# Kernel tuning notes

Hardware: AMD Instinct MI355X
Metric: run time of the kernel (lower is better)

The kernel has to match this reference:

```python
import jax, jax.numpy as jnp
import numpy as np
from math import ceil

B, N, C_IN, H, EDIM = 64, 512, 128, 128, 5
EPG = 16 * N          # edges per graph
E = B * EPG           # 524288 edges total
K1 = ceil(0.5 * N)    # 256 clusters after pool 1
K2 = ceil(0.5 * K1)   # 128 clusters after pool 2
EPS = 1e-15


def dense_mincut_pool(x, adj, s, mask=None):
    # x: [B,n,F], adj: [B,n,n], s: [B,n,k]
    s = jax.nn.softmax(s, axis=-1)
    if mask is not None:
        m = mask[..., None].astype(x.dtype)
        x = x * m
        s = s * m
    out = jnp.einsum('bnk,bnf->bkf', s, x)
    out_adj = jnp.einsum('bnk,bnm,bml->bkl', s, adj, s)
    mincut_num = jnp.trace(out_adj, axis1=-2, axis2=-1)
    d_flat = adj.sum(-1)                                   # degrees [B,n]
    mincut_den = jnp.trace(jnp.einsum('bnk,bn,bnl->bkl', s, d_flat, s), axis1=-2, axis2=-1)
    mincut_loss = jnp.mean(-(mincut_num / mincut_den))
    k = s.shape[-1]
    ss = jnp.einsum('bnk,bnl->bkl', s, s)
    ss_norm = jnp.linalg.norm(ss, axis=(-1, -2), keepdims=True)
    i_s = jnp.eye(k, dtype=x.dtype)
    ortho_loss = jnp.mean(jnp.linalg.norm(ss / ss_norm - i_s / np.sqrt(k), axis=(-1, -2)))
    out_adj = out_adj * (1.0 - i_s)                        # zero diagonal
    d = jnp.sqrt(out_adj.sum(-1))[..., None] + EPS
    out_adj = out_adj / d / jnp.swapaxes(d, -1, -2)
    return out, out_adj, mincut_loss, ortho_loss


def setup_inputs() -> dict:
    key = jax.random.key(0)
    ks = iter(jax.random.split(key, 40))
    NT = B * N
    x = jax.random.normal(next(ks), (NT, C_IN), jnp.float32)
    # within-graph random edges; nodes are sorted by graph (batch = repeat)
    offs = jnp.repeat(jnp.arange(B, dtype=jnp.int32) * N, EPG)
    src = jax.random.randint(next(ks), (E,), 0, N, jnp.int32) + offs
    dst = jax.random.randint(next(ks), (E,), 0, N, jnp.int32) + offs
    edge_index = jnp.stack([src, dst])
    edge_attr = jax.random.normal(next(ks), (E, EDIM), jnp.float32)
    batch = jnp.repeat(jnp.arange(B, dtype=jnp.int32), N)

    def W(shape):
        return jax.random.normal(next(ks), shape, jnp.float32) * 0.05

    inp = dict(x=x, edge_index=edge_index, edge_attr=edge_attr, batch=batch,
               bn_gamma=jnp.ones((C_IN,), jnp.float32), bn_beta=jnp.zeros((C_IN,), jnp.float32),
               Wq=W((C_IN, H)), bq=W((H,)), Wk=W((C_IN, H)), bk=W((H,)),
               Wv=W((C_IN, H)), bv=W((H,)), We=W((EDIM, H)),
               Wskip=W((C_IN, H)), bskip=W((H,)),
               W_mlp1=W((H, K1)), b_mlp1=W((K1,)),
               W2_rel=W((H, H)), b2_rel=W((H,)), W2_root=W((H, H)),
               W_mlp2=W((H, K2)), b_mlp2=W((K2,)),
               W3_rel=W((H, H)), b3_rel=W((H,)), W3_root=W((H, H)),
               W_lin1=W((H, H)), b_lin1=W((H,)),
               W_ro=W((H, 1)), b_ro=W((1,)))
    return inp


def reference(x, edge_index, edge_attr, batch, bn_gamma, bn_beta,
              Wq, bq, Wk, bk, Wv, bv, We, Wskip, bskip,
              W_mlp1, b_mlp1, W2_rel, b2_rel, W2_root,
              W_mlp2, b_mlp2, W3_rel, b3_rel, W3_root,
              W_lin1, b_lin1, W_ro, b_ro):
    NT = x.shape[0]
    # BatchNorm1d (training-mode batch statistics, biased var, eps=1e-5)
    mu = x.mean(0)
    var = x.var(0)
    xh = (x - mu) / jnp.sqrt(var + 1e-5) * bn_gamma + bn_beta

    # TransformerConv (heads=1, concat=True, root_weight=True, edge_dim=5)
    src, dst = edge_index[0], edge_index[1]
    q = xh @ Wq + bq
    k_ = xh @ Wk + bk
    v = xh @ Wv + bv
    e = edge_attr @ We                       # lin_edge has no bias
    kj = k_[src] + e
    vj = v[src] + e
    logits = (q[dst] * kj).sum(-1) / np.sqrt(H)
    m = jax.ops.segment_max(logits, dst, num_segments=NT)
    a = jnp.exp(logits - m[dst])
    denom = jax.ops.segment_sum(a, dst, num_segments=NT)
    alpha = a / denom[dst]
    agg = jax.ops.segment_sum(alpha[:, None] * vj, dst, num_segments=NT)
    h = jax.nn.relu(agg + xh @ Wskip + bskip)

    # to_dense_batch: equal-size graphs sorted by batch -> reshape
    xd = h.reshape(B, N, H)
    mask = jnp.ones((B, N), bool)
    # to_dense_adj: scatter-add edge indicators (duplicates accumulate)
    adj = jnp.zeros((B, N, N), jnp.float32).at[batch[src], src % N, dst % N].add(1.0)

    s = xd @ W_mlp1 + b_mlp1
    xd, adj, mc1, o1 = dense_mincut_pool(xd, adj, s, mask)
    # DenseGraphConv: lin_rel(adj @ x) + lin_root(x)
    xd = jax.nn.relu((adj @ xd) @ W2_rel + b2_rel + xd @ W2_root)
    s = xd @ W_mlp2 + b_mlp2
    xd, adj, mc2, o2 = dense_mincut_pool(xd, adj, s)
    xd = (adj @ xd) @ W3_rel + b3_rel + xd @ W3_root
    g = xd.mean(1)
    g = jax.nn.relu(g @ W_lin1 + b_lin1)
    return jax.nn.sigmoid(g @ W_ro + b_ro).squeeze(-1)   # [B]
```

## Files before the change

kernel.cpp:

```cpp
#include <hip/hip_runtime.h>
#include <math.h>

#define BGRAPH 64
#define NNODE  512
#define NTOT   32768
#define CIN    128
#define HDIM   128
#define EDIM_  5
#define EDGES  524288
#define K1C    256
#define K2C    128

using f32x4 = __attribute__((ext_vector_type(4))) float;
using s16x8 = __attribute__((ext_vector_type(8))) short;

__device__ __forceinline__ short f2bf(float f) {
    union { float f; unsigned u; } v; v.f = f;
    unsigned r = v.u + 0x7fffu + ((v.u >> 16) & 1u);
    return (short)(r >> 16);
}
__device__ __forceinline__ float bf2f(short s) {
    union { unsigned u; float f; } v; v.u = ((unsigned)(unsigned short)s) << 16;
    return v.f;
}

__global__ __launch_bounds__(256) void prep_kernel(const float* __restrict__ x,
                                                   float* __restrict__ psum,
                                                   float* __restrict__ psq,
                                                   const float* __restrict__ Wq, const float* __restrict__ Wk,
                                                   const float* __restrict__ Wv, const float* __restrict__ Ws,
                                                   const float* __restrict__ bq, const float* __restrict__ bk,
                                                   const float* __restrict__ bv, const float* __restrict__ bs,
                                                   float* __restrict__ W4, float* __restrict__ bias4,
                                                   const int* __restrict__ ei,
                                                   int* __restrict__ deg_src,
                                                   int* __restrict__ deg_dst) {
    __shared__ float ss[128], sq[128];
    int tid = threadIdx.x, bid = blockIdx.x;
    if (bid < 256) {
        long idx0 = (long)bid * 256 + tid;
        float4 s = {0.f, 0.f, 0.f, 0.f}, q = {0.f, 0.f, 0.f, 0.f};
#pragma unroll
        for (int it = 0; it < 16; ++it) {
            float4 v = *(const float4*)(x + (idx0 + (long)it * 65536) * 4);
            s.x += v.x; s.y += v.y; s.z += v.z; s.w += v.w;
            q.x += v.x * v.x; q.y += v.y * v.y; q.z += v.z * v.z; q.w += v.w * v.w;
        }
        if (tid < 128) { ss[tid] = 0.f; sq[tid] = 0.f; }
        __syncthreads();
        int c0 = (tid & 31) * 4;
        atomicAdd(&ss[c0 + 0], s.x); atomicAdd(&ss[c0 + 1], s.y);
        atomicAdd(&ss[c0 + 2], s.z); atomicAdd(&ss[c0 + 3], s.w);
        atomicAdd(&sq[c0 + 0], q.x); atomicAdd(&sq[c0 + 1], q.y);
        atomicAdd(&sq[c0 + 2], q.z); atomicAdd(&sq[c0 + 3], q.w);
        __syncthreads();
        if (tid < 128) {
            psum[bid * 128 + tid] = ss[tid];
            psq[bid * 128 + tid]  = sq[tid];
        }
    } else if (bid < 512) {
        int i = (bid - 256) * 256 + tid;
        if (i < 128 * 512) {
            int k = i / 512, j = i % 512;
            float v;
            if (j < 128)      v = Wq[k * 128 + j];
            else if (j < 256) v = Wk[k * 128 + (j - 128)];
            else if (j < 384) v = Wv[k * 128 + (j - 256)];
            else              v = Ws[k * 128 + (j - 384)];
            W4[i] = v;
        }
        if (i < 512) {
            float v;
            if (i < 128)      v = bq[i];
            else if (i < 256) v = bk[i - 128];
            else if (i < 384) v = bv[i - 256];
            else              v = bs[i - 384];
            bias4[i] = v;
        }
    } else {
        int e = (bid - 512) * 256 + tid;
        if (e < EDGES) {
            atomicAdd(&deg_src[ei[e]], 1);
            atomicAdd(&deg_dst[ei[EDGES + e]], 1);
        }
    }
}

__global__ __launch_bounds__(1024) void scan2fin_kernel(const int* __restrict__ deg_src,
                                                        int* __restrict__ rp_src, int* __restrict__ cur_src,
                                                        const int* __restrict__ deg_dst,
                                                        int* __restrict__ rp_dst, int* __restrict__ cur_dst,
                                                        const float* __restrict__ psum,
                                                        const float* __restrict__ psq,
                                                        const float* __restrict__ gamma,
                                                        const float* __restrict__ beta,
                                                        float* __restrict__ scale,
                                                        float* __restrict__ shift,
                                                        float* __restrict__ gsum) {
    __shared__ int part[1024];
    int tid = threadIdx.x;
    if (blockIdx.x == 2) {
        if (tid < 128) {
            int c = tid;
            float s = 0.f, q = 0.f;
            for (int b = 0; b < 256; ++b) { s += psum[b * 128 + c]; q += psq[b * 128 + c]; }
            float mu  = s / (float)NTOT;
            float var = q / (float)NTOT - mu * mu;
            float rstd = rsqrtf(var + 1e-5f);
            float sc = gamma[c] * rstd;
            scale[c] = sc;
            shift[c] = beta[c] - mu * sc;
        }
        for (int i = tid; i < BGRAPH * 128; i += 1024) gsum[i] = 0.f;
        return;
    }
    const int* deg = blockIdx.x ? deg_dst : deg_src;
    int* rowptr    = blockIdx.x ? rp_dst  : rp_src;
    int* cursor    = blockIdx.x ? cur_dst : cur_src;
    int base = tid * 32;
    int s = 0;
    for (int i = 0; i < 32; ++i) s += deg[base + i];
    part[tid] = s;
    __syncthreads();
    for (int off = 1; off < 1024; off <<= 1) {
        int v = part[tid];
        int add = (tid >= off) ? part[tid - off] : 0;
        __syncthreads();
        part[tid] = v + add;
        __syncthreads();
    }
    int run = (tid == 0) ? 0 : part[tid - 1];
    for (int i = 0; i < 32; ++i) {
        rowptr[base + i] = run;
        cursor[base + i] = run;
        run += deg[base + i];
    }
}

template <int TILE, bool TRANS_A, bool AFFINE, bool ANORM, bool ROWSUM, bool RELU,
          bool DUAL, bool OBF16, bool AU8, bool BBF16, bool ATRBF16, bool ABF16>
__device__ __forceinline__ void mgemm_body(short* As, short* Bs, float* dvl,
                                           const void* __restrict__ Av,
                                           const void* __restrict__ Bv,
                                           const void* __restrict__ A2v,
                                           const void* __restrict__ B2v,
                                           int Ksplit,
                                           const float* __restrict__ bias,
                                           void* __restrict__ Cv,
                                           const float* __restrict__ scale,
                                           const float* __restrict__ shift,
                                           int M, int Nc, int K,
                                           int lda, int ldb, int ldc,
                                           long sA, long sB, long sC,
                                           int bx, int by, int bz) {
    constexpr int ASZ = AU8 ? 1 : ((ATRBF16 || ABF16) ? 2 : 4);
    constexpr int BSZ = BBF16 ? 2 : 4;
    const char* Abase = (const char*)Av + (long)bz * sA * ASZ;
    const char* Bbase = (const char*)Bv + (long)bz * sB * BSZ;
    float* C = (float*)Cv + (OBF16 ? 0 : (long)bz * sC);
    short* Cs = (short*)Cv + (OBF16 ? (long)bz * sC : 0);
    const int m0 = by * TILE, n0 = bx * TILE;
    const int tid = threadIdx.x;
    const int lane16 = tid & 15;
    const int quad = (tid & 63) >> 4;
    const int wrow = (tid >> 6) >> 1, wcol = (tid >> 6) & 1;
    constexpr int WT = TILE / 32;

    if (ANORM) {
        for (int i = tid; i < K; i += 256)
            dvl[i] = 1.f / (sqrtf(scale[(long)bz * lda + i]) + 1e-15f);
        __syncthreads();
    }

    f32x4 acc[WT][WT] = {};

    for (int k0 = 0; k0 < K; k0 += 32) {
        const char* Au = Abase; const char* Bu = Bbase; int ku = k0;
        if (DUAL && k0 >= Ksplit) { Au = (const char*)A2v; Bu = (const char*)B2v; ku = k0 - Ksplit; }

        if (!TRANS_A) {
#pragma unroll
            for (int p = 0; p < TILE / 32; ++p) {
                int idx = tid + p * 256;
                int row = idx >> 3, c4 = idx & 7;
                short4 o;
                if (AU8) {
                    unsigned u = *(const unsigned*)((const unsigned char*)Au +
                                                    (long)(m0 + row) * lda + ku + c4 * 4);
                    o = make_short4(f2bf((float)(u & 255u)), f2bf((float)((u >> 8) & 255u)),
                                    f2bf((float)((u >> 16) & 255u)), f2bf((float)((u >> 24) & 255u)));
                } else if (ABF16) {
                    o = *(const short4*)((const short*)Au + (long)(m0 + row) * lda + ku + c4 * 4);
                } else {
                    float4 v = *(const float4*)((const float*)Au + (long)(m0 + row) * lda + ku + c4 * 4);
                    if (AFFINE) {
                        int k = ku + c4 * 4;
                        v.x = v.x * scale[k] + shift[k];
                        v.y = v.y * scale[k + 1] + shift[k + 1];
                        v.z = v.z * scale[k + 2] + shift[k + 2];
                        v.w = v.w * scale[k + 3] + shift[k + 3];
                    }
                    if (ANORM) {
                        int k = ku + c4 * 4;
                        int grow = m0 + row;
                        float dr = dvl[grow];
                        v.x = (grow == k + 0) ? 0.f : v.x * dr * dvl[k + 0];
                        v.y = (grow == k + 1) ? 0.f : v.y * dr * dvl[k + 1];
                        v.z = (grow == k + 2) ? 0.f : v.z * dr * dvl[k + 2];
                        v.w = (grow == k + 3) ? 0.f : v.w * dr * dvl[k + 3];
                    }
                    o = make_short4(f2bf(v.x), f2bf(v.y), f2bf(v.z), f2bf(v.w));
                }
                *(short4*)&As[row * 40 + c4 * 4] = o;
            }
        } else {
            if (TILE == 128 || tid < 128) {
                int c4 = tid >> 3, g = tid & 7;
                short* d = &As[(c4 * 4) * 40 + g * 4];
                if (ATRBF16) {
                    const short* src = (const short*)Au + (long)(ku + g * 4) * lda + m0 + c4 * 4;
                    short4 r0 = *(const short4*)(src);
                    short4 r1 = *(const short4*)(src + lda);
                    short4 r2 = *(const short4*)(src + 2 * lda);
                    short4 r3 = *(const short4*)(src + 3 * lda);
                    *(short4*)(d + 0 * 40) = make_short4(r0.x, r1.x, r2.x, r3.x);
                    *(short4*)(d + 1 * 40) = make_short4(r0.y, r1.y, r2.y, r3.y);
                    *(short4*)(d + 2 * 40) = make_short4(r0.z, r1.z, r2.z, r3.z);
                    *(short4*)(d + 3 * 40) = make_short4(r0.w, r1.w, r2.w, r3.w);
                } else {
                    const float* src = (const float*)Au + (long)(ku + g * 4) * lda + m0 + c4 * 4;
                    float4 r0 = *(const float4*)(src);
                    float4 r1 = *(const float4*)(src + lda);
                    float4 r2 = *(const float4*)(src + 2 * lda);
                    float4 r3 = *(const float4*)(src + 3 * lda);
                    *(short4*)(d + 0 * 40) = make_short4(f2bf(r0.x), f2bf(r1.x), f2bf(r2.x), f2bf(r3.x));
                    *(short4*)(d + 1 * 40) = make_short4(f2bf(r0.y), f2bf(r1.y), f2bf(r2.y), f2bf(r3.y));
                    *(short4*)(d + 2 * 40) = make_short4(f2bf(r0.z), f2bf(r1.z), f2bf(r2.z), f2bf(r3.z));
                    *(short4*)(d + 3 * 40) = make_short4(f2bf(r0.w), f2bf(r1.w), f2bf(r2.w), f2bf(r3.w));
                }
            }
        }
        if (TILE == 128 || tid < 128) {
            int c4 = tid >> 3, g = tid & 7;
            short* d = &Bs[(c4 * 4) * 40 + g * 4];
            if (BBF16) {
                const short* src = (const short*)Bu + (long)(ku + g * 4) * ldb + n0 + c4 * 4;
                short4 r0 = *(const short4*)(src);
                short4 r1 = *(const short4*)(src + ldb);
                short4 r2 = *(const short4*)(src + 2 * ldb);
                short4 r3 = *(const short4*)(src + 3 * ldb);
                *(short4*)(d + 0 * 40) = make_short4(r0.x, r1.x, r2.x, r3.x);
                *(short4*)(d + 1 * 40) = make_short4(r0.y, r1.y, r2.y, r3.y);
                *(short4*)(d + 2 * 40) = make_short4(r0.z, r1.z, r2.z, r3.z);
                *(short4*)(d + 3 * 40) = make_short4(r0.w, r1.w, r2.w, r3.w);
            } else {
                const float* src = (const float*)Bu + (long)(ku + g * 4) * ldb + n0 + c4 * 4;
                float4 r0 = *(const float4*)(src);
                float4 r1 = *(const float4*)(src + ldb);
                float4 r2 = *(const float4*)(src + 2 * ldb);
                float4 r3 = *(const float4*)(src + 3 * ldb);
                *(short4*)(d + 0 * 40) = make_short4(f2bf(r0.x), f2bf(r1.x), f2bf(r2.x), f2bf(r3.x));
                *(short4*)(d + 1 * 40) = make_short4(f2bf(r0.y), f2bf(r1.y), f2bf(r2.y), f2bf(r3.y));
                *(short4*)(d + 2 * 40) = make_short4(f2bf(r0.z), f2bf(r1.z), f2bf(r2.z), f2bf(r3.z));
                *(short4*)(d + 3 * 40) = make_short4(f2bf(r0.w), f2bf(r1.w), f2bf(r2.w), f2bf(r3.w));
            }
        }
        __syncthreads();

        s16x8 af[WT], bf[WT];
#pragma unroll
        for (int t = 0; t < WT; ++t) {
            af[t] = *(const s16x8*)&As[(wrow * (TILE / 2) + t * 16 + lane16) * 40 + quad * 8];
            bf[t] = *(const s16x8*)&Bs[(wcol * (TILE / 2) + t * 16 + lane16) * 40 + quad * 8];
        }
#pragma unroll
        for (int i = 0; i < WT; ++i)
#pragma unroll
            for (int j = 0; j < WT; ++j)
                acc[i][j] = __builtin_amdgcn_mfma_f32_16x16x32_bf16(af[i], bf[j], acc[i][j], 0, 0, 0);
        __syncthreads();
    }

#pragma unroll
    for (int i = 0; i < WT; ++i) {
        int gm = m0 + wrow * (TILE / 2) + i * 16 + quad * 4;
#pragma unroll
        for (int j = 0; j < WT; ++j) {
            int gn = n0 + wcol * (TILE / 2) + j * 16 + lane16;
            float bv = bias ? bias[gn] : 0.f;
#pragma unroll
            for (int r = 0; r < 4; ++r) {
                float val = acc[i][j][r] + bv;
                if (RELU) val = fmaxf(val, 0.f);
                if (OBF16) Cs[(long)(gm + r) * ldc + gn] = f2bf(val);
                else       C[(long)(gm + r) * ldc + gn] = val;
            }
        }
    }

    if (ROWSUM) {
        float* rlA = (float*)As;
        float* rlB = (float*)Bs;
#pragma unroll
        for (int i = 0; i < WT; ++i) {
#pragma unroll
            for (int r = 0; r < 4; ++r) {
                int gm = m0 + wrow * (TILE / 2) + i * 16 + quad * 4 + r;
                float p = 0.f;
#pragma unroll
                for (int j = 0; j < WT; ++j) {
                    int gn = n0 + wcol * (TILE / 2) + j * 16 + lane16;
                    p += (gn == gm) ? 0.f : acc[i][j][r];
                }
#pragma unroll
                for (int off = 1; off < 16; off <<= 1) p += __shfl_xor(p, off);
                if (lane16 == 0) {
                    int rl = wrow * (TILE / 2) + i * 16 + quad * 4 + r;
                    (wcol ? rlB : rlA)[rl] = p;
                }
            }
        }
        __syncthreads();
        float* rout = (float*)shift;
        for (int t = tid; t < TILE; t += 256)
            atomicAdd(&rout[(long)bz * M + m0 + t], rlA[t] + rlB[t]);
    }
}

template <int TILE, bool TRANS_A, bool AFFINE, bool ANORM, bool ROWSUM, bool RELU,
          bool DUAL, bool OBF16, bool AU8, bool BBF16, bool ATRBF16, bool ABF16>
__global__ __launch_bounds__(256) void mgemm(const void* __restrict__ Av,
                                             const void* __restrict__ Bv,
                                             const void* __restrict__ A2v,
                                             const void* __restrict__ B2v,
                                             int Ksplit,
                                             const float* __restrict__ bias,
                                             void* __restrict__ Cv,
                                             const float* __restrict__ scale,
                                             const float* __restrict__ shift,
                                             int M, int Nc, int K,
                                             int lda, int ldb, int ldc,
                                             long sA, long sB, long sC) {
    __shared__ __align__(16) short As[TILE * 40];
    __shared__ __align__(16) short Bs[TILE * 40];
    __shared__ float dvl[ANORM ? 256 : 1];
    mgemm_body<TILE, TRANS_A, AFFINE, ANORM, ROWSUM, RELU, DUAL, OBF16, AU8, BBF16, ATRBF16, ABF16>(
        As, Bs, dvl, Av, Bv, A2v, B2v, Ksplit, bias, Cv, scale, shift,
        M, Nc, K, lda, ldb, ldc, sA, sB, sC,
        blockIdx.x, blockIdx.y, blockIdx.z);
}

__global__ __launch_bounds__(256) void qkvs_scatter_kernel(const float* __restrict__ x,
                                                           const float* __restrict__ W4,
                                                           const float* __restrict__ bias4,
                                                           short* __restrict__ qkvs,
                                                           const float* __restrict__ scale,
                                                           const float* __restrict__ shift,
                                                           const int* __restrict__ ei,
                                                           int* __restrict__ cur_src,
                                                           int* __restrict__ cur_dst,
                                                           int* __restrict__ eid_src,
                                                           int* __restrict__ eid_dst) {
    __shared__ __align__(16) short As[128 * 40];
    __shared__ __align__(16) short Bs[128 * 40];
    int b = blockIdx.x;
    if (b < 1024) {
        mgemm_body<128, false, true, false, false, false, false, true, false, false, false, false>(
            As, Bs, nullptr, x, W4, nullptr, nullptr, 0, bias4, qkvs, scale, shift,
            NTOT, 512, 128, 128, 512, 512, 0, 0, 0,
            b & 3, b >> 2, 0);
    } else {
        int e = (b - 1024) * 256 + threadIdx.x;
        if (e < EDGES) {
            int s = ei[e], d = ei[EDGES + e];
            eid_src[atomicAdd(&cur_src[s], 1)] = e;
            eid_dst[atomicAdd(&cur_dst[d], 1)] = e;
        }
    }
}

__global__ __launch_bounds__(256) void pool1_kernel(const short* __restrict__ s1b,
                                                    const short* __restrict__ h,
                                                    const short* __restrict__ T1s,
                                                    float* __restrict__ xp1,
                                                    float* __restrict__ adj1,
                                                    float* __restrict__ rowsum1) {
    __shared__ __align__(16) short As[128 * 40];
    __shared__ __align__(16) short Bs[128 * 40];
    int b = blockIdx.x;
    if (b < 512) {
        mgemm_body<64, true, false, false, false, false, false, false, false, true, true, false>(
            As, Bs, nullptr, s1b, h, nullptr, nullptr, 0, nullptr, xp1, nullptr, nullptr,
            K1C, 128, NNODE, K1C, 128, 128,
            (long)NNODE * K1C, (long)NNODE * 128, (long)K1C * 128,
            b & 1, (b >> 1) & 3, b >> 3);
    } else {
        int j = b - 512;
        mgemm_body<128, true, false, false, true, false, false, false, false, true, true, false>(
            As, Bs, nullptr, s1b, T1s, nullptr, nullptr, 0, nullptr, adj1, nullptr, rowsum1,
            K1C, K1C, NNODE, K1C, K1C, K1C,
            (long)NNODE * K1C, (long)NNODE * K1C, (long)K1C * K1C,
            j & 1, (j >> 1) & 1, j >> 2);
    }
}

__global__ __launch_bounds__(256) void pool2_kernel(const float* __restrict__ adj1,
                                                    const float* __restrict__ rowsum1,
                                                    const short* __restrict__ s2b,
                                                    const short* __restrict__ xd2,
                                                    float* __restrict__ t2,
                                                    float* __restrict__ xp2) {
    __shared__ __align__(16) short As[64 * 40];
    __shared__ __align__(16) short Bs[64 * 40];
    __shared__ float dvl[256];
    int b = blockIdx.x;
    if (b < 512) {
        mgemm_body<64, false, false, true, false, false, false, false, false, true, false, false>(
            As, Bs, dvl, adj1, s2b, nullptr, nullptr, 0, nullptr, t2, rowsum1, nullptr,
            K1C, K2C, K1C, K1C, K2C, K2C,
            (long)K1C * K1C, (long)K1C * K2C, (long)K1C * K2C,
            b & 1, (b >> 1) & 3, b >> 3);
    } else {
        int j = b - 512;
        mgemm_body<64, true, false, false, false, false, false, false, false, true, true, false>(
            As, Bs, nullptr, s2b, xd2, nullptr, nullptr, 0, nullptr, xp2, nullptr, nullptr,
            K2C, 128, K1C, K2C, 128, 128,
            (long)K1C * K2C, (long)K1C * 128, (long)K2C * 128,
            j & 1, (j >> 1) & 1, j >> 2);
    }
}

template <int KADJ, bool RELU, bool OBF16, bool COLSUM>
__global__ __launch_bounds__(256) void fused_gc_kernel(const float* __restrict__ adj,
                                                       const float* __restrict__ rowsum,
                                                       const float* __restrict__ xp,
                                                       const float* __restrict__ Wrel,
                                                       const float* __restrict__ brel,
                                                       const float* __restrict__ Wroot,
                                                       void* __restrict__ Outv) {
    __shared__ __align__(16) short As[64 * 40];
    __shared__ __align__(16) short Bs[128 * 40];
    __shared__ __align__(16) short Tl[64][136];
    __shared__ float dvl[KADJ];
    __shared__ float cs[COLSUM ? 128 : 1];
    const int z = blockIdx.y;
    const int m0 = blockIdx.x * 64;
    const int tid = threadIdx.x;
    const int lane16 = tid & 15;
    const int quad = (tid & 63) >> 4;
    const int wrow = (tid >> 6) >> 1, wcol = (tid >> 6) & 1;
    const float* adjz = adj + (long)z * KADJ * KADJ;
    const float* xpz  = xp + (long)z * KADJ * 128;

    for (int i = tid; i < KADJ; i += 256)
        dvl[i] = 1.f / (sqrtf(rowsum[(long)z * KADJ + i]) + 1e-15f);
    if (COLSUM) for (int i = tid; i < 128; i += 256) cs[i] = 0.f;
    __syncthreads();

    f32x4 acc[2][4] = {};
    for (int k0 = 0; k0 < KADJ; k0 += 32) {
#pragma unroll
        for (int p = 0; p < 2; ++p) {
            int idx = tid + p * 256;
            int row = idx >> 3, c4 = idx & 7;
            int grow = m0 + row, k = k0 + c4 * 4;
            float4 v = *(const float4*)(adjz + (long)grow * KADJ + k);
            float dr = dvl[grow];
            v.x = (grow == k + 0) ? 0.f : v.x * dr * dvl[k + 0];
            v.y = (grow == k + 1) ? 0.f : v.y * dr * dvl[k + 1];
            v.z = (grow == k + 2) ? 0.f : v.z * dr * dvl[k + 2];
            v.w = (grow == k + 3) ? 0.f : v.w * dr * dvl[k + 3];
            *(short4*)&As[row * 40 + c4 * 4] =
                make_short4(f2bf(v.x), f2bf(v.y), f2bf(v.z), f2bf(v.w));
        }
        {
            int c4 = tid >> 3, g = tid & 7;
            short* d = &Bs[(c4 * 4) * 40 + g * 4];
            const float* src = xpz + (long)(k0 + g * 4) * 128 + c4 * 4;
            float4 r0 = *(const float4*)(src);
            float4 r1 = *(const float4*)(src + 128);
            float4 r2 = *(const float4*)(src + 256);
            float4 r3 = *(const float4*)(src + 384);
            *(short4*)(d + 0 * 40) = make_short4(f2bf(r0.x), f2bf(r1.x), f2bf(r2.x), f2bf(r3.x));
            *(short4*)(d + 1 * 40) = make_short4(f2bf(r0.y), f2bf(r1.y), f2bf(r2.y), f2bf(r3.y));
            *(short4*)(d + 2 * 40) = make_short4(f2bf(r0.z), f2bf(r1.z), f2bf(r2.z), f2bf(r3.z));
            *(short4*)(d + 3 * 40) = make_short4(f2bf(r0.w), f2bf(r1.w), f2bf(r2.w), f2bf(r3.w));
        }
        __syncthreads();
        s16x8 af[2], bf[4];
#pragma unroll
        for (int t = 0; t < 2; ++t)
            af[t] = *(const s16x8*)&As[(wrow * 32 + t * 16 + lane16) * 40 + quad * 8];
#pragma unroll
        for (int j = 0; j < 4; ++j)
            bf[j] = *(const s16x8*)&Bs[(wcol * 64 + j * 16 + lane16) * 40 + quad * 8];
#pragma unroll
        for (int t = 0; t < 2; ++t)
#pragma unroll
            for (int j = 0; j < 4; ++j)
                acc[t][j] = __builtin_amdgcn_mfma_f32_16x16x32_bf16(af[t], bf[j], acc[t][j], 0, 0, 0);
        __syncthreads();
    }
#pragma unroll
    for (int t = 0; t < 2; ++t)
#pragma unroll
        for (int j = 0; j < 4; ++j)
#pragma unroll
            for (int r = 0; r < 4; ++r)
                Tl[wrow * 32 + t * 16 + quad * 4 + r][wcol * 64 + j * 16 + lane16] =
                    f2bf(acc[t][j][r]);
    __syncthreads();

    f32x4 acc2[2][4] = {};
    for (int k0 = 0; k0 < 256; k0 += 32) {
        const bool useXp = (k0 >= 128);
        const float* Wsrc = useXp ? (Wroot + (long)(k0 - 128) * 128)
                                  : (Wrel + (long)k0 * 128);
        {
            int c4 = tid >> 3, g = tid & 7;
            short* d = &Bs[(c4 * 4) * 40 + g * 4];
            const float* src = Wsrc + (long)(g * 4) * 128 + c4 * 4;
            float4 r0 = *(const float4*)(src);
            float4 r1 = *(const float4*)(src + 128);
            float4 r2 = *(const float4*)(src + 256);
            float4 r3 = *(const float4*)(src + 384);
            *(short4*)(d + 0 * 40) = make_short4(f2bf(r0.x), f2bf(r1.x), f2bf(r2.x), f2bf(r3.x));
            *(short4*)(d + 1 * 40) = make_short4(f2bf(r0.y), f2bf(r1.y), f2bf(r2.y), f2bf(r3.y));
            *(short4*)(d + 2 * 40) = make_short4(f2bf(r0.z), f2bf(r1.z), f2bf(r2.z), f2bf(r3.z));
            *(short4*)(d + 3 * 40) = make_short4(f2bf(r0.w), f2bf(r1.w), f2bf(r2.w), f2bf(r3.w));
        }
        if (useXp) {
#pragma unroll
            for (int p = 0; p < 2; ++p) {
                int idx = tid + p * 256;
                int row = idx >> 3, c4 = idx & 7;
                float4 v = *(const float4*)(xpz + (long)(m0 + row) * 128 + (k0 - 128) + c4 * 4);
                *(short4*)&As[row * 40 + c4 * 4] =
                    make_short4(f2bf(v.x), f2bf(v.y), f2bf(v.z), f2bf(v.w));
            }
        }
        __syncthreads();
        s16x8 af[2], bf[4];
#pragma unroll
        for (int t = 0; t < 2; ++t) {
            int ar = wrow * 32 + t * 16 + lane16;
            af[t] = useXp ? *(const s16x8*)&As[ar * 40 + quad * 8]
                          : *(const s16x8*)&Tl[ar][k0 + quad * 8];
        }
#pragma unroll
        for (int j = 0; j < 4; ++j)
            bf[j] = *(const s16x8*)&Bs[(wcol * 64 + j * 16 + lane16) * 40 + quad * 8];
#pragma unroll
        for (int t = 0; t < 2; ++t)
#pragma unroll
            for (int j = 0; j < 4; ++j)
                acc2[t][j] = __builtin_amdgcn_mfma_f32_16x16x32_bf16(af[t], bf[j], acc2[t][j], 0, 0, 0);
        __syncthreads();
    }

    if (!COLSUM) {
        float* Of = (float*)Outv;
        short* Ob = (short*)Outv;
#pragma unroll
        for (int t = 0; t < 2; ++t) {
#pragma unroll
            for (int j = 0; j < 4; ++j) {
                int gcol = wcol * 64 + j * 16 + lane16;
                float bv = brel[gcol];
#pragma unroll
                for (int r = 0; r < 4; ++r) {
                    int grow = m0 + wrow * 32 + t * 16 + quad * 4 + r;
                    float val = acc2[t][j][r] + bv;
                    if (RELU) val = fmaxf(val, 0.f);
                    long oi = ((long)z * KADJ + grow) * 128 + gcol;
                    if (OBF16) Ob[oi] = f2bf(val);
                    else       Of[oi] = val;
                }
            }
        }
    } else {
#pragma unroll
        for (int j = 0; j < 4; ++j) {
            int gcol = wcol * 64 + j * 16 + lane16;
            float bv = brel[gcol];
            float p = 0.f;
#pragma unroll
            for (int t = 0; t < 2; ++t)
#pragma unroll
                for (int r = 0; r < 4; ++r) {
                    float val = acc2[t][j][r] + bv;
                    if (RELU) val = fmaxf(val, 0.f);
                    p += val;
                }
            atomicAdd(&cs[gcol], p);
        }
        __syncthreads();
        float* gsum = (float*)Outv;
        for (int i = tid; i < 128; i += 256)
            atomicAdd(&gsum[(long)z * 128 + i], cs[i]);
    }
}

template <int NC>
__global__ __launch_bounds__(256) void mlp_softmax_kernel(const short* __restrict__ A,
                                                          const float* __restrict__ W,
                                                          const float* __restrict__ bias,
                                                          short* __restrict__ Out) {
    __shared__ __align__(16) short As[64 * 40];
    __shared__ __align__(16) short Ws[NC * 40];
    const int tid = threadIdx.x;
    const int lane16 = tid & 15;
    const int quad = (tid & 63) >> 4;
    const int wv = tid >> 6;
    const int m0 = blockIdx.x * 64;
    constexpr int NT = NC / 16;

    f32x4 acc[NT] = {};

    for (int k0 = 0; k0 < 128; k0 += 32) {
        {
            int row = tid >> 2, g = tid & 3;
            *(s16x8*)&As[row * 40 + g * 8] =
                *(const s16x8*)(A + (long)(m0 + row) * 128 + k0 + g * 8);
        }
#pragma unroll
        for (int p = 0; p < NC / 128; ++p) {
            int c4 = tid >> 3, g = tid & 7;
            int n0 = p * 128 + c4 * 4;
            short* d = &Ws[n0 * 40 + g * 4];
            const float* src = W + (long)(k0 + g * 4) * NC + n0;
            float4 r0 = *(const float4*)(src);
            float4 r1 = *(const float4*)(src + NC);
            float4 r2 = *(const float4*)(src + 2 * NC);
            float4 r3 = *(const float4*)(src + 3 * NC);
            *(short4*)(d + 0 * 40) = make_short4(f2bf(r0.x), f2bf(r1.x), f2bf(r2.x), f2bf(r3.x));
            *(short4*)(d + 1 * 40) = make_short4(f2bf(r0.y), f2bf(r1.y), f2bf(r2.y), f2bf(r3.y));
            *(short4*)(d + 2 * 40) = make_short4(f2bf(r0.z), f2bf(r1.z), f2bf(r2.z), f2bf(r3.z));
            *(short4*)(d + 3 * 40) = make_short4(f2bf(r0.w), f2bf(r1.w), f2bf(r2.w), f2bf(r3.w));
        }
        __syncthreads();

        s16x8 af = *(const s16x8*)&As[(wv * 16 + lane16) * 40 + quad * 8];
#pragma unroll
        for (int t = 0; t < NT; ++t) {
            s16x8 bf = *(const s16x8*)&Ws[(t * 16 + lane16) * 40 + quad * 8];
            acc[t] = __builtin_amdgcn_mfma_f32_16x16x32_bf16(af, bf, acc[t], 0, 0, 0);
        }
        __syncthreads();
    }

    float mx[4] = {-INFINITY, -INFINITY, -INFINITY, -INFINITY};
#pragma unroll
    for (int t = 0; t < NT; ++t) {
        float bv = bias[t * 16 + lane16];
#pragma unroll
        for (int r = 0; r < 4; ++r) {
            float x = bf2f(f2bf(acc[t][r] + bv));
            acc[t][r] = x;
            mx[r] = fmaxf(mx[r], x);
        }
    }
#pragma unroll
    for (int off = 8; off; off >>= 1)
#pragma unroll
        for (int r = 0; r < 4; ++r) mx[r] = fmaxf(mx[r], __shfl_xor(mx[r], off));
    float sm[4] = {0.f, 0.f, 0.f, 0.f};
#pragma unroll
    for (int t = 0; t < NT; ++t)
#pragma unroll
        for (int r = 0; r < 4; ++r) {
            float e = expf(acc[t][r] - mx[r]);
            acc[t][r] = e;
            sm[r] += e;
        }
#pragma unroll
    for (int off = 8; off; off >>= 1)
#pragma unroll
        for (int r = 0; r < 4; ++r) sm[r] += __shfl_xor(sm[r], off);
#pragma unroll
    for (int r = 0; r < 4; ++r) sm[r] = 1.f / sm[r];
#pragma unroll
    for (int t = 0; t < NT; ++t)
#pragma unroll
        for (int r = 0; r < 4; ++r)
            Out[(long)(m0 + wv * 16 + quad * 4 + r) * NC + t * 16 + lane16] =
                f2bf(acc[t][r] * sm[r]);
}

template <bool OBF16>
__global__ __launch_bounds__(256) void bgemm(const short* __restrict__ A,
                                             const short* __restrict__ B,
                                             void* __restrict__ Cv,
                                             float outscale,
                                             int M, int Nc, int K,
                                             int lda, int ldb, int ldc,
                                             long sA, long sB, long sC) {
    __shared__ __align__(16) short As[128 * 40];
    __shared__ __align__(16) short Bs[128 * 40];
    int L = blockIdx.x + (blockIdx.y << 2) + (blockIdx.z << 4);
    int xcd = L & 7, i = L >> 3;
    const int z = xcd * 8 + (i >> 4);
    const int m0 = ((i >> 2) & 3) * 128, n0 = (i & 3) * 128;
    A += (long)z * sA;
    B += (long)z * sB;
    float* C = (float*)Cv + (OBF16 ? 0 : (long)z * sC);
    short* Cs = (short*)Cv + (OBF16 ? (long)z * sC : 0);
    const int tid = threadIdx.x;
    const int lane16 = tid & 15;
    const int quad = (tid & 63) >> 4;
    const int wrow = (tid >> 6) >> 1, wcol = (tid >> 6) & 1;

    f32x4 acc[4][4] = {};

    for (int k0 = 0; k0 < K; k0 += 32) {
#pragma unroll
        for (int p = 0; p < 2; ++p) {
            int u = tid + p * 256;
            int row = u >> 2, g = u & 3;
            *(s16x8*)&As[row * 40 + g * 8] =
                *(const s16x8*)(A + (long)(m0 + row) * lda + k0 + g * 8);
        }
#pragma unroll
        for (int p = 0; p < 2; ++p) {
            int u = tid + p * 256;
            int row = u >> 2, g = u & 3;
            *(s16x8*)&Bs[row * 40 + g * 8] =
                *(const s16x8*)(B + (long)(n0 + row) * ldb + k0 + g * 8);
        }
        __syncthreads();

        s16x8 af[4], bf[4];
#pragma unroll
        for (int t = 0; t < 4; ++t) {
            af[t] = *(const s16x8*)&As[(wrow * 64 + t * 16 + lane16) * 40 + quad * 8];
            bf[t] = *(const s16x8*)&Bs[(wcol * 64 + t * 16 + lane16) * 40 + quad * 8];
        }
#pragma unroll
        for (int i2 = 0; i2 < 4; ++i2)
#pragma unroll
            for (int j = 0; j < 4; ++j)
                acc[i2][j] = __builtin_amdgcn_mfma_f32_16x16x32_bf16(af[i2], bf[j], acc[i2][j], 0, 0, 0);
        __syncthreads();
    }

#pragma unroll
    for (int i2 = 0; i2 < 4; ++i2) {
        int gm = m0 + wrow * 64 + i2 * 16 + quad * 4;
#pragma unroll
        for (int j = 0; j < 4; ++j) {
            int gn = n0 + wcol * 64 + j * 16 + lane16;
#pragma unroll
            for (int r = 0; r < 4; ++r) {
                float val = acc[i2][j][r] * outscale;
                if (OBF16) Cs[(long)(gm + r) * ldc + gn] = f2bf(val);
                else       C[(long)(gm + r) * ldc + gn] = val;
            }
        }
    }
}

__global__ __launch_bounds__(256) void attn_pv_kernel(const short* __restrict__ S,
                                                      const int* __restrict__ ei,
                                                      const float* __restrict__ eattr,
                                                      const float* __restrict__ We,
                                                      const int* __restrict__ rp_dst,
                                                      const int* __restrict__ deg_dst,
                                                      const int* __restrict__ eid_dst,
                                                      const short* __restrict__ qkvs,
                                                      float* __restrict__ alpha,
                                                      short* __restrict__ h) {
    __shared__ float sWe[EDIM_ * 128];
    __shared__ __align__(16) short sS[16][528];
    int g = threadIdx.x >> 4;
    int lane = threadIdx.x & 15;
    int gbase = (threadIdx.x & 63) & ~15;
    int b = blockIdx.x;
    int xcd = b & 7, idx = b >> 3;
    int nb = (xcd * 8 + (idx >> 5)) * 32 + (idx & 31);
    int node = nb * 16 + g;

    {
        const short* Srow = S + (long)node * 512;
        short* Sl = sS[g];
#pragma unroll
        for (int j = 0; j < 4; ++j)
            *(s16x8*)&Sl[j * 128 + lane * 8] = *(const s16x8*)(Srow + j * 128 + lane * 8);
    }
    for (int i = threadIdx.x; i < EDIM_ * 128; i += 256) sWe[i] = We[i];
    __syncthreads();
    const short* Sl = sS[g];

    float qw[EDIM_];
    {
        s16x8 qv = *(const s16x8*)(qkvs + (long)node * 512 + lane * 8);
        float qf[8];
#pragma unroll
        for (int j = 0; j < 8; ++j) qf[j] = bf2f(qv[j]);
#pragma unroll
        for (int d = 0; d < EDIM_; ++d) {
            float p = 0.f;
#pragma unroll
            for (int j = 0; j < 8; ++j) p += qf[j] * sWe[d * 128 + lane * 8 + j];
            qw[d] = p;
        }
#pragma unroll
        for (int off = 8; off; off >>= 1)
#pragma unroll
            for (int d = 0; d < EDIM_; ++d) qw[d] += __shfl_xor(qw[d], off);
#pragma unroll
        for (int d = 0; d < EDIM_; ++d) qw[d] *= 0.08838834764831845f;
    }

    int start = rp_dst[node], cnt = deg_dst[node];
    int nch = (cnt + 15) >> 4;

    float lsum = 0.f, a5[EDIM_] = {};
    int   src_c[4] = {0, 0, 0, 0};
    float a_c[4]   = {0.f, 0.f, 0.f, 0.f};
    for (int c = 0; c < nch; ++c) {
        int t = c * 16 + lane;
        int src = 0; float wv = 0.f;
        if (t < cnt) {
            int e = eid_dst[start + t];
            src = ei[e];
            float lg = bf2f(Sl[src & 511]);
            float ea[EDIM_];
#pragma unroll
            for (int d = 0; d < EDIM_; ++d) { ea[d] = eattr[e * EDIM_ + d]; lg += ea[d] * qw[d]; }
            wv = expf(lg);
            lsum += wv;
#pragma unroll
            for (int d = 0; d < EDIM_; ++d) a5[d] += wv * ea[d];
        }
        if (c < 4) { src_c[c] = src; a_c[c] = wv; }
        else if (t < cnt) alpha[start + t] = wv;
    }
#pragma unroll
    for (int off = 8; off; off >>= 1) {
        lsum += __shfl_xor(lsum, off);
#pragma unroll
        for (int d = 0; d < EDIM_; ++d) a5[d] += __shfl_xor(a5[d], off);
    }
    float inv = (lsum > 0.f) ? 1.f / lsum : 0.f;
    float e5[EDIM_];
#pragma unroll
    for (int d = 0; d < EDIM_; ++d) e5[d] = a5[d] * inv;

    float acc[8] = {};
    for (int c = 0; c < nch; ++c) {
        int src; float a;
        if (c < 4) { src = src_c[c]; a = a_c[c]; }
        else {
            int t = c * 16 + lane;
            if (t < cnt) {
                int e = eid_dst[start + t];
                src = ei[e];
                a = alpha[start + t];
            } else { src = 0; a = 0.f; }
        }
        int m = min(16, cnt - c * 16);
        if (m == 16) {
#pragma unroll
            for (int j = 0; j < 16; ++j) {
                int   sj = __shfl(src, gbase + j);
                float aj = __shfl(a,   gbase + j);
                s16x8 v = *(const s16x8*)(qkvs + (long)sj * 512 + 256 + lane * 8);
#pragma unroll
                for (int k = 0; k < 8; ++k) acc[k] += aj * bf2f(v[k]);
            }
        } else {
            for (int j = 0; j < m; ++j) {
                int   sj = __shfl(src, gbase + j);
                float aj = __shfl(a,   gbase + j);
                s16x8 v = *(const s16x8*)(qkvs + (long)sj * 512 + 256 + lane * 8);
#pragma unroll
                for (int k = 0; k < 8; ++k) acc[k] += aj * bf2f(v[k]);
            }
        }
    }

    s16x8 sk = *(const s16x8*)(qkvs + (long)node * 512 + 384 + lane * 8);
    s16x8 o;
#pragma unroll
    for (int j = 0; j < 8; ++j) {
        float ec = 0.f;
#pragma unroll
        for (int d = 0; d < EDIM_; ++d) ec += e5[d] * sWe[d * 128 + lane * 8 + j];
        float val = acc[j] * inv + ec + bf2f(sk[j]);
        o[j] = f2bf(fmaxf(val, 0.f));
    }
    *(s16x8*)(h + (long)node * 128 + lane * 8) = o;
}

__global__ __launch_bounds__(256) void t1_gather_kernel(const int* __restrict__ ei,
                                                        const int* __restrict__ rp_src,
                                                        const int* __restrict__ deg_src,
                                                        const int* __restrict__ eid_src,
                                                        const short* __restrict__ s1b,
                                                        short* __restrict__ T1s) {
    int g = threadIdx.x >> 4;
    int lane = threadIdx.x & 15;
    int gbase = (threadIdx.x & 63) & ~15;
    int b = blockIdx.x;
    int xcd = b & 7, idx = b >> 3;
    int nb = (xcd * 8 + (idx >> 5)) * 32 + (idx & 31);
    int node = nb * 16 + g;

    int start = rp_src[node], cnt = deg_src[node];
    int nch = (cnt + 15) >> 4;
    float acc[16] = {};
    for (int c = 0; c < nch; ++c) {
        int t = c * 16 + lane;
        int dst = 0;
        if (t < cnt) {
            int e = eid_src[start + t];
            dst = ei[EDGES + e];
        }
        int m = min(16, cnt - c * 16);
        if (m == 16) {
#pragma unroll
            for (int j = 0; j < 16; ++j) {
                int dj = __shfl(dst, gbase + j);
                const s16x8* p = (const s16x8*)(s1b + (long)dj * 256 + lane * 16);
                s16x8 v0 = p[0], v1 = p[1];
#pragma unroll
                for (int k = 0; k < 8; ++k) { acc[k] += bf2f(v0[k]); acc[8 + k] += bf2f(v1[k]); }
            }
        } else {
            for (int j = 0; j < m; ++j) {
                int dj = __shfl(dst, gbase + j);
                const s16x8* p = (const s16x8*)(s1b + (long)dj * 256 + lane * 16);
                s16x8 v0 = p[0], v1 = p[1];
#pragma unroll
                for (int k = 0; k < 8; ++k) { acc[k] += bf2f(v0[k]); acc[8 + k] += bf2f(v1[k]); }
            }
        }
    }
    s16x8 o0, o1;
#pragma unroll
    for (int k = 0; k < 8; ++k) { o0[k] = f2bf(acc[k]); o1[k] = f2bf(acc[8 + k]); }
    short* o = T1s + (long)node * 256 + lane * 16;
    *(s16x8*)(o)     = o0;
    *(s16x8*)(o + 8) = o1;
}

__global__ __launch_bounds__(128) void readout_kernel(const float* __restrict__ gsum,
                                                      const float* __restrict__ W_lin1,
                                                      const float* __restrict__ b_lin1,
                                                      const float* __restrict__ W_ro,
                                                      const float* __restrict__ b_ro,
                                                      float* __restrict__ out) {
    int b = blockIdx.x, t = threadIdx.x;
    __shared__ float g[128], g2[128], wred[2];
    g[t] = gsum[(long)b * 128 + t] * (1.f / (float)K2C);
    __syncthreads();
    float u = b_lin1[t];
    for (int k = 0; k < 128; ++k) u += g[k] * W_lin1[k * 128 + t];
    g2[t] = fmaxf(u, 0.f);
    __syncthreads();
    float p = g2[t] * W_ro[t];
#pragma unroll
    for (int off = 32; off; off >>= 1) p += __shfl_xor(p, off);
    if ((t & 63) == 0) wred[t >> 6] = p;
    __syncthreads();
    if (t == 0) {
        float tot = wred[0] + wred[1] + b_ro[0];
        out[b] = 1.f / (1.f + expf(-tot));
    }
}

extern "C" void kernel_launch(void* const* d_in, const int* in_sizes, int n_in,
                              void* d_out, int out_size, void* d_ws, size_t ws_size,
                              hipStream_t stream) {
    const float* x      = (const float*)d_in[0];
    const int*   ei     = (const int*)d_in[1];
    const float* eattr  = (const float*)d_in[2];
    const float* gamma  = (const float*)d_in[4];
    const float* beta   = (const float*)d_in[5];
    const float* Wq     = (const float*)d_in[6];
    const float* bq     = (const float*)d_in[7];
    const float* Wk     = (const float*)d_in[8];
    const float* bk     = (const float*)d_in[9];
    const float* Wv     = (const float*)d_in[10];
    const float* bv     = (const float*)d_in[11];
    const float* We     = (const float*)d_in[12];
    const float* Wskip  = (const float*)d_in[13];
    const float* bskip  = (const float*)d_in[14];
    const float* W_mlp1 = (const float*)d_in[15];
    const float* b_mlp1 = (const float*)d_in[16];
    const float* W2_rel = (const float*)d_in[17];
    const float* b2_rel = (const float*)d_in[18];
    const float* W2_root= (const float*)d_in[19];
    const float* W_mlp2 = (const float*)d_in[20];
    const float* b_mlp2 = (const float*)d_in[21];
    const float* W3_rel = (const float*)d_in[22];
    const float* b3_rel = (const float*)d_in[23];
    const float* W3_root= (const float*)d_in[24];
    const float* W_lin1 = (const float*)d_in[25];
    const float* b_lin1 = (const float*)d_in[26];
    const float* W_ro   = (const float*)d_in[27];
    const float* b_ro   = (const float*)d_in[28];
    float* out = (float*)d_out;

    char* w = (char*)d_ws;
    const size_t MB = 1ull << 20;
    short* qkvs = (short*)(w + 0);
    short* S    = (short*)(w + 32 * MB);
    short* T1s  = (short*)(w + 48 * MB);
    short* s1b  = (short*)(w + 64 * MB);
    short* xd2  = (short*)(w + 56 * MB);
    short* s2b  = (short*)(w + 72 * MB);
    float* t2   = (float*)(w + 64 * MB);
    float* adj2 = (float*)(w + 0);
    float* xp2  = (float*)(w + 4 * MB);
    float* adj1 = (float*)(w + 80 * MB);
    float* xp1  = (float*)(w + 96 * MB);
    float* alpha= (float*)(w + 97 * MB);
    short* h    = (short*)(w + 112 * MB);
    char* misc  = w + 104 * MB;
    float* W4     = (float*)(misc + 0x00000);
    float* bias4  = (float*)(misc + 0x40000);
    float* scale  = (float*)(misc + 0x41400);
    float* shift  = (float*)(misc + 0x41600);
    float* rowsum1= (float*)(misc + 0x42000);
    float* rowsum2= (float*)(misc + 0x52000);
    int* deg_src  = (int*)(misc + 0x60000);
    int* deg_dst  = (int*)(misc + 0x80000);
    int* rp_src   = (int*)(misc + 0xA0000);
    int* rp_dst   = (int*)(misc + 0xC0000);
    int* cur_src  = (int*)(misc + 0xE0000);
    int* cur_dst  = (int*)(misc + 0x100000);
    int* eid_src  = (int*)(misc + 0x120000);
    int* eid_dst  = (int*)(misc + 0x320000);
    float* psum   = (float*)(misc + 0x520000);
    float* psq    = (float*)(misc + 0x540000);
    float* gsum   = (float*)(misc + 0x560000);

    hipMemsetAsync(misc + 0x42000, 0, 0xA0000 - 0x42000, stream);

    prep_kernel<<<2560, 256, 0, stream>>>(x, psum, psq,
                                          Wq, Wk, Wv, Wskip, bq, bk, bv, bskip,
                                          W4, bias4, ei, deg_src, deg_dst);

    scan2fin_kernel<<<3, 1024, 0, stream>>>(deg_src, rp_src, cur_src,
                                            deg_dst, rp_dst, cur_dst,
                                            psum, psq, gamma, beta, scale, shift, gsum);

    qkvs_scatter_kernel<<<3072, 256, 0, stream>>>(x, W4, bias4, qkvs, scale, shift,
                                                  ei, cur_src, cur_dst, eid_src, eid_dst);

    bgemm<true><<<dim3(4, 4, BGRAPH), 256, 0, stream>>>(
        qkvs + 0, qkvs + 128, S, 0.08838834764831845f,
        NNODE, NNODE, 128, 512, 512, 512,
        (long)NNODE * 512, (long)NNODE * 512, (long)NNODE * NNODE);

    attn_pv_kernel<<<NTOT / 16, 256, 0, stream>>>(
        S, ei, eattr, We, rp_dst, deg_dst, eid_dst, qkvs, alpha, h);

    mlp_softmax_kernel<K1C><<<NTOT / 64, 256, 0, stream>>>(h, W_mlp1, b_mlp1, s1b);

    t1_gather_kernel<<<NTOT / 16, 256, 0, stream>>>(
        ei, rp_src, deg_src, eid_src, s1b, T1s);

    pool1_kernel<<<768, 256, 0, stream>>>(s1b, h, T1s, xp1, adj1, rowsum1);

    fused_gc_kernel<K1C, true, true, false><<<dim3(4, BGRAPH), 256, 0, stream>>>(
        adj1, rowsum1, xp1, W2_rel, b2_rel, W2_root, xd2);

    mlp_softmax_kernel<K2C><<<(BGRAPH * K1C) / 64, 256, 0, stream>>>(xd2, W_mlp2, b_mlp2, s2b);

    pool2_kernel<<<768, 256, 0, stream>>>(adj1, rowsum1, s2b, xd2, t2, xp2);

    mgemm<64, true, false, false, true, false, false, false, false, false, true, false>
        <<<dim3(2, 2, BGRAPH), 256, 0, stream>>>(
        s2b, t2, nullptr, nullptr, 0, nullptr, adj2, nullptr, rowsum2,
        K2C, K2C, K1C, K2C, K2C, K2C,
        (long)K1C * K2C, (long)K1C * K2C, (long)K2C * K2C);

    fused_gc_kernel<K2C, false, false, true><<<dim3(2, BGRAPH), 256, 0, stream>>>(
        adj2, rowsum2, xp2, W3_rel, b3_rel, W3_root, gsum);

    readout_kernel<<<BGRAPH, 128, 0, stream>>>(gsum, W_lin1, b_lin1, W_ro, b_ro, out);

    (void)in_sizes; (void)n_in; (void)out_size; (void)ws_size;
}
```

Measured before the change: 444.5 us.

## Build per-graph CSR in shared memory instead of global atomics and scans

Removes the global degree-count atomics, the global prefix-scan kernel and the global cursor atomics used to build src/dst CSR. Each graph's edges are now bucketed in one block, using shared-memory counting, a block scan and a local scatter, and this work runs alongside the QKVS GEMM blocks. This relies on edges being contiguous per graph with nodes local to each graph, and it changes edge ordering within each row to a nondeterministic one. It also shrinks the memset and the prep grid.

```diff
diff --git a/kernel.cpp b/kernel.cpp
--- a/kernel.cpp
+++ b/kernel.cpp
@@ -8,6 +8,7 @@
 #define HDIM   128
 #define EDIM_  5
 #define EDGES  524288
+#define EPG    8192
 #define K1C    256
 #define K2C    128
 
@@ -31,10 +32,7 @@
                                                    const float* __restrict__ Wv, const float* __restrict__ Ws,
                                                    const float* __restrict__ bq, const float* __restrict__ bk,
                                                    const float* __restrict__ bv, const float* __restrict__ bs,
-                                                   float* __restrict__ W4, float* __restrict__ bias4,
-                                                   const int* __restrict__ ei,
-                                                   int* __restrict__ deg_src,
-                                                   int* __restrict__ deg_dst) {
+                                                   float* __restrict__ W4, float* __restrict__ bias4) {
     __shared__ float ss[128], sq[128];
     int tid = threadIdx.x, bid = blockIdx.x;
     if (bid < 256) {
@@ -58,7 +56,7 @@
             psum[bid * 128 + tid] = ss[tid];
             psq[bid * 128 + tid]  = sq[tid];
         }
-    } else if (bid < 512) {
+    } else {
         int i = (bid - 256) * 256 + tid;
         if (i < 128 * 512) {
             int k = i / 512, j = i % 512;
@@ -77,64 +75,29 @@
             else              v = bs[i - 384];
             bias4[i] = v;
         }
-    } else {
-        int e = (bid - 512) * 256 + tid;
-        if (e < EDGES) {
-            atomicAdd(&deg_src[ei[e]], 1);
-            atomicAdd(&deg_dst[ei[EDGES + e]], 1);
-        }
-    }
-}
-
-__global__ __launch_bounds__(1024) void scan2fin_kernel(const int* __restrict__ deg_src,
-                                                        int* __restrict__ rp_src, int* __restrict__ cur_src,
-                                                        const int* __restrict__ deg_dst,
-                                                        int* __restrict__ rp_dst, int* __restrict__ cur_dst,
-                                                        const float* __restrict__ psum,
-                                                        const float* __restrict__ psq,
-                                                        const float* __restrict__ gamma,
-                                                        const float* __restrict__ beta,
-                                                        float* __restrict__ scale,
-                                                        float* __restrict__ shift,
-                                                        float* __restrict__ gsum) {
-    __shared__ int part[1024];
+    }
+}
+
+__global__ __launch_bounds__(1024) void fin_kernel(const float* __restrict__ psum,
+                                                   const float* __restrict__ psq,
+                                                   const float* __restrict__ gamma,
+                                                   const float* __restrict__ beta,
+                                                   float* __restrict__ scale,
+                                                   float* __restrict__ shift,
+                                                   float* __restrict__ gsum) {
     int tid = threadIdx.x;
-    if (blockIdx.x == 2) {
-        if (tid < 128) {
-            int c = tid;
-            float s = 0.f, q = 0.f;
-            for (int b = 0; b < 256; ++b) { s += psum[b * 128 + c]; q += psq[b * 128 + c]; }
-            float mu  = s / (float)NTOT;
-            float var = q / (float)NTOT - mu * mu;
-            float rstd = rsqrtf(var + 1e-5f);
-            float sc = gamma[c] * rstd;
-            scale[c] = sc;
-            shift[c] = beta[c] - mu * sc;
-        }
-        for (int i = tid; i < BGRAPH * 128; i += 1024) gsum[i] = 0.f;
-        return;
-    }
-    const int* deg = blockIdx.x ? deg_dst : deg_src;
-    int* rowptr    = blockIdx.x ? rp_dst  : rp_src;
-    int* cursor    = blockIdx.x ? cur_dst : cur_src;
-    int base = tid * 32;
-    int s = 0;
-    for (int i = 0; i < 32; ++i) s += deg[base + i];
-    part[tid] = s;
-    __syncthreads();
-    for (int off = 1; off < 1024; off <<= 1) {
-        int v = part[tid];
-        int add = (tid >= off) ? part[tid - off] : 0;
-        __syncthreads();
-        part[tid] = v + add;
-        __syncthreads();
-    }
-    int run = (tid == 0) ? 0 : part[tid - 1];
-    for (int i = 0; i < 32; ++i) {
-        rowptr[base + i] = run;
-        cursor[base + i] = run;
-        run += deg[base + i];
-    }
+    if (tid < 128) {
+        int c = tid;
+        float s = 0.f, q = 0.f;
+        for (int b = 0; b < 256; ++b) { s += psum[b * 128 + c]; q += psq[b * 128 + c]; }
+        float mu  = s / (float)NTOT;
+        float var = q / (float)NTOT - mu * mu;
+        float rstd = rsqrtf(var + 1e-5f);
+        float sc = gamma[c] * rstd;
+        scale[c] = sc;
+        shift[c] = beta[c] - mu * sc;
+    }
+    for (int i = tid; i < BGRAPH * 128; i += 1024) gsum[i] = 0.f;
 }
 
 template <int TILE, bool TRANS_A, bool AFFINE, bool ANORM, bool ROWSUM, bool RELU,
@@ -350,32 +313,82 @@
         blockIdx.x, blockIdx.y, blockIdx.z);
 }
 
-__global__ __launch_bounds__(256) void qkvs_scatter_kernel(const float* __restrict__ x,
-                                                           const float* __restrict__ W4,
-                                                           const float* __restrict__ bias4,
-                                                           short* __restrict__ qkvs,
-                                                           const float* __restrict__ scale,
-                                                           const float* __restrict__ shift,
-                                                           const int* __restrict__ ei,
-                                                           int* __restrict__ cur_src,
-                                                           int* __restrict__ cur_dst,
-                                                           int* __restrict__ eid_src,
-                                                           int* __restrict__ eid_dst) {
-    __shared__ __align__(16) short As[128 * 40];
-    __shared__ __align__(16) short Bs[128 * 40];
+__device__ __forceinline__ void csr_build_graph(int* smemInt,
+                                                const int* __restrict__ ei_dir,
+                                                int gnode0, int gedge0,
+                                                int* __restrict__ rp,
+                                                int* __restrict__ deg,
+                                                int* __restrict__ eid) {
+    int* cnt  = smemInt;
+    int* part = smemInt + 512;
+    int* eidl = smemInt + 768;
+    int tid = threadIdx.x;
+    cnt[tid] = 0; cnt[tid + 256] = 0;
+    __syncthreads();
+    for (int k = 0; k < EPG / 256; ++k) {
+        int e = gedge0 + k * 256 + tid;
+        atomicAdd(&cnt[ei_dir[e] & 511], 1);
+    }
+    __syncthreads();
+    int c0 = cnt[2 * tid], c1 = cnt[2 * tid + 1];
+    part[tid] = c0 + c1;
+    __syncthreads();
+    for (int off = 1; off < 256; off <<= 1) {
+        int v = part[tid];
+        int add = (tid >= off) ? part[tid - off] : 0;
+        __syncthreads();
+        part[tid] = v + add;
+        __syncthreads();
+    }
+    int excl = (tid == 0) ? 0 : part[tid - 1];
+    rp[gnode0 + 2 * tid]      = gedge0 + excl;
+    rp[gnode0 + 2 * tid + 1]  = gedge0 + excl + c0;
+    deg[gnode0 + 2 * tid]     = c0;
+    deg[gnode0 + 2 * tid + 1] = c1;
+    cnt[2 * tid]     = excl;
+    cnt[2 * tid + 1] = excl + c0;
+    __syncthreads();
+    for (int k = 0; k < EPG / 256; ++k) {
+        int e = gedge0 + k * 256 + tid;
+        int pos = atomicAdd(&cnt[ei_dir[e] & 511], 1);
+        eidl[pos] = e;
+    }
+    __syncthreads();
+    for (int k = 0; k < EPG / 256; ++k)
+        eid[gedge0 + k * 256 + tid] = eidl[k * 256 + tid];
+}
+
+__global__ __launch_bounds__(256) void qkvs_csr_kernel(const float* __restrict__ x,
+                                                       const float* __restrict__ W4,
+                                                       const float* __restrict__ bias4,
+                                                       short* __restrict__ qkvs,
+                                                       const float* __restrict__ scale,
+                                                       const float* __restrict__ shift,
+                                                       const int* __restrict__ ei,
+                                                       int* __restrict__ rp_src,
+                                                       int* __restrict__ deg_src,
+                                                       int* __restrict__ eid_src,
+                                                       int* __restrict__ rp_dst,
+                                                       int* __restrict__ deg_dst,
+                                                       int* __restrict__ eid_dst) {
+    __shared__ __align__(16) char smem[35840];
     int b = blockIdx.x;
     if (b < 1024) {
+        short* As = (short*)smem;
+        short* Bs = (short*)(smem + 10240);
         mgemm_body<128, false, true, false, false, false, false, true, false, false, false, false>(
             As, Bs, nullptr, x, W4, nullptr, nullptr, 0, bias4, qkvs, scale, shift,
             NTOT, 512, 128, 128, 512, 512, 0, 0, 0,
             b & 3, b >> 2, 0);
     } else {
-        int e = (b - 1024) * 256 + threadIdx.x;
-        if (e < EDGES) {
-            int s = ei[e], d = ei[EDGES + e];
-            eid_src[atomicAdd(&cur_src[s], 1)] = e;
-            eid_dst[atomicAdd(&cur_dst[d], 1)] = e;
-        }
+        int j = b - 1024;
+        int g = j >> 1;
+        if (j & 1)
+            csr_build_graph((int*)smem, ei + EDGES, g * NNODE, g * EPG,
+                            rp_dst, deg_dst, eid_dst);
+        else
+            csr_build_graph((int*)smem, ei, g * NNODE, g * EPG,
+                            rp_src, deg_src, eid_src);
     }
 }
 
@@ -1028,26 +1041,23 @@
     int* deg_dst  = (int*)(misc + 0x80000);
     int* rp_src   = (int*)(misc + 0xA0000);
     int* rp_dst   = (int*)(misc + 0xC0000);
-    int* cur_src  = (int*)(misc + 0xE0000);
-    int* cur_dst  = (int*)(misc + 0x100000);
     int* eid_src  = (int*)(misc + 0x120000);
     int* eid_dst  = (int*)(misc + 0x320000);
     float* psum   = (float*)(misc + 0x520000);
     float* psq    = (float*)(misc + 0x540000);
     float* gsum   = (float*)(misc + 0x560000);
 
-    hipMemsetAsync(misc + 0x42000, 0, 0xA0000 - 0x42000, stream);
-
-    prep_kernel<<<2560, 256, 0, stream>>>(x, psum, psq,
-                                          Wq, Wk, Wv, Wskip, bq, bk, bv, bskip,
-                                          W4, bias4, ei, deg_src, deg_dst);
-
-    scan2fin_kernel<<<3, 1024, 0, stream>>>(deg_src, rp_src, cur_src,
-                                            deg_dst, rp_dst, cur_dst,
-                                            psum, psq, gamma, beta, scale, shift, gsum);
-
-    qkvs_scatter_kernel<<<3072, 256, 0, stream>>>(x, W4, bias4, qkvs, scale, shift,
-                                                  ei, cur_src, cur_dst, eid_src, eid_dst);
+    hipMemsetAsync(misc + 0x42000, 0, 0x18000, stream);
+
+    prep_kernel<<<512, 256, 0, stream>>>(x, psum, psq,
+                                         Wq, Wk, Wv, Wskip, bq, bk, bv, bskip,
+                                         W4, bias4);
+
+    fin_kernel<<<1, 1024, 0, stream>>>(psum, psq, gamma, beta, scale, shift, gsum);
+
+    qkvs_csr_kernel<<<1152, 256, 0, stream>>>(x, W4, bias4, qkvs, scale, shift,
+                                              ei, rp_src, deg_src, eid_src,
+                                              rp_dst, deg_dst, eid_dst);
 
     bgemm<true><<<dim3(4, 4, BGRAPH), 256, 0, stream>>>(
         qkvs + 0, qkvs + 128, S, 0.08838834764831845f,
```

New measurement: 411.7 us (median of 2 runs). 7.4% less time.
